# Kernel optimization log

Measured on AMD Instinct MI355X. Metric: run time of the kernel, lower is better.

Reference implementation:

```python
import jax, jax.numpy as jnp
import numpy as np
from jax import lax


def _lstm_layer(x, Wih, Whh, bih, bhh):
    # x: [B, T, D_in]; PyTorch gate order: i, f, g, o. Returns all hidden states [B, T, H].
    B = x.shape[0]
    H = Whh.shape[1]
    bias = bih + bhh
    # Precompute input projections for all timesteps: [T, B, 4H]
    xg = jnp.einsum('btd,gd->tbg', x, Wih) + bias

    def step(carry, xg_t):
        h, c = carry
        gates = xg_t + h @ Whh.T  # [B, 4H]
        i, f, g, o = jnp.split(gates, 4, axis=-1)
        i = jax.nn.sigmoid(i)
        f = jax.nn.sigmoid(f)
        g = jnp.tanh(g)
        o = jax.nn.sigmoid(o)
        c = f * c + i * g
        h = o * jnp.tanh(c)
        return (h, c), h

    h0 = jnp.zeros((B, H), dtype=x.dtype)
    c0 = jnp.zeros((B, H), dtype=x.dtype)
    (_, _), hs = lax.scan(step, (h0, c0), xg)  # hs: [T, B, H]
    return hs.transpose(1, 0, 2)


def setup_inputs() -> dict:
    key = jax.random.key(0)
    ks = jax.random.split(key, 13)
    B, T, D = 4096, 128, 32
    H1, H2 = 64, 32
    s = lambda n: 1.0 / np.sqrt(n)
    return {
        'x': jax.random.normal(ks[0], (B, T, D), jnp.float32),
        'Wih1': jax.random.uniform(ks[1], (4 * H1, D), jnp.float32, -s(H1), s(H1)),
        'Whh1': jax.random.uniform(ks[2], (4 * H1, H1), jnp.float32, -s(H1), s(H1)),
        'bih1': jax.random.uniform(ks[3], (4 * H1,), jnp.float32, -s(H1), s(H1)),
        'bhh1': jax.random.uniform(ks[4], (4 * H1,), jnp.float32, -s(H1), s(H1)),
        'Wih2': jax.random.uniform(ks[5], (4 * H2, H1), jnp.float32, -s(H2), s(H2)),
        'Whh2': jax.random.uniform(ks[6], (4 * H2, H2), jnp.float32, -s(H2), s(H2)),
        'bih2': jax.random.uniform(ks[7], (4 * H2,), jnp.float32, -s(H2), s(H2)),
        'bhh2': jax.random.uniform(ks[8], (4 * H2,), jnp.float32, -s(H2), s(H2)),
        'fc1_w': jax.random.uniform(ks[9], (16, H2), jnp.float32, -s(H2), s(H2)),
        'fc1_b': jax.random.uniform(ks[10], (16,), jnp.float32, -s(H2), s(H2)),
        'fc2_w': jax.random.uniform(ks[11], (1, 16), jnp.float32, -0.25, 0.25),
        'fc2_b': jax.random.uniform(ks[12], (1,), jnp.float32, -0.25, 0.25),
    }


def reference(x, Wih1, Whh1, bih1, bhh1, Wih2, Whh2, bih2, bhh2, fc1_w, fc1_b, fc2_w, fc2_b):
    out = _lstm_layer(x, Wih1, Whh1, bih1, bhh1)        # [B, T, H1]; dropout = identity (eval)
    out = _lstm_layer(out, Wih2, Whh2, bih2, bhh2)       # [B, T, H2]
    last = out[:, -1, :]                                  # [B, H2]
    h = jax.nn.relu(last @ fc1_w.T + fc1_b)               # [B, 16]
    return h @ fc2_w.T + fc2_b                            # [B, 1]
```

## Files before the change

kernel.cpp:

```cpp
#include <hip/hip_runtime.h>


constexpr int Tt      = 128;
constexpr int NB      = 8;
constexpr int THREADS = 256;

struct __align__(16) Smem {
  float scr[8192];
  float h1t[2][64][12];
  float h2t[2][32][12];
  float xs [2][32][12];
};

static_assert(sizeof(Smem) <= 80 * 1024, "need 2 blocks/CU");

__device__ __forceinline__ float frcp(float x)   { return __builtin_amdgcn_rcpf(x); }
__device__ __forceinline__ float fsig(float x)   { return frcp(1.0f + __expf(-x)); }
__device__ __forceinline__ float ftanh_(float x) { return 1.0f - 2.0f * frcp(1.0f + __expf(2.0f * x)); }

template<int P>
__device__ __forceinline__ float swz(float v) {
  return __int_as_float(__builtin_amdgcn_ds_swizzle(__float_as_int(v), P));
}

__global__ __launch_bounds__(THREADS, 2)
void lstm_fused(const float* __restrict__ x,
                const float* __restrict__ Wih1, const float* __restrict__ Whh1,
                const float* __restrict__ bih1, const float* __restrict__ bhh1,
                const float* __restrict__ Wih2, const float* __restrict__ Whh2,
                const float* __restrict__ bih2, const float* __restrict__ bhh2,
                const float* __restrict__ fc1w, const float* __restrict__ fc1b,
                const float* __restrict__ fc2w, const float* __restrict__ fc2b,
                float* __restrict__ out)
{
  __shared__ Smem s;
  const int tid = threadIdx.x;
  const int b0  = blockIdx.x * NB;

  const int ks1 = tid & 3;
  const int u1  = tid >> 2;
  const int ks2 = tid & 7;
  const int u2  = tid >> 3;

  float w1[24][4];
  float w2[12][4];

  auto stage = [&](const float* g, int n) {
    for (int e = tid * 4; e < n; e += THREADS * 4)
      *(float4*)&s.scr[e] = *(const float4*)&g[e];
  };

  stage(Wih1, 8192);
  __syncthreads();
#pragma unroll
  for (int j = 0; j < 8; ++j)
#pragma unroll
    for (int g = 0; g < 4; ++g)
      w1[j][g] = s.scr[(g * 64 + u1) * 32 + ks1 + 4 * j];
  __syncthreads();

  stage(Whh1, 8192);
  __syncthreads();
#pragma unroll
  for (int j = 8; j < 24; ++j)
#pragma unroll
    for (int g = 0; g < 2; ++g)
      w1[j][g] = s.scr[(g * 64 + u1) * 64 + ks1 + 4 * (j - 8)];
  __syncthreads();

  stage(Whh1 + 8192, 8192);
  __syncthreads();
#pragma unroll
  for (int j = 8; j < 24; ++j)
#pragma unroll
    for (int g = 2; g < 4; ++g)
      w1[j][g] = s.scr[((g - 2) * 64 + u1) * 64 + ks1 + 4 * (j - 8)];
  __syncthreads();

  stage(Wih2, 8192);
  __syncthreads();
#pragma unroll
  for (int j = 0; j < 8; ++j)
#pragma unroll
    for (int g = 0; g < 4; ++g)
      w2[j][g] = s.scr[(g * 32 + u2) * 64 + ks2 + 8 * j];
  __syncthreads();

  stage(Whh2, 4096);
  __syncthreads();
#pragma unroll
  for (int j = 8; j < 12; ++j)
#pragma unroll
    for (int g = 0; g < 4; ++g)
      w2[j][g] = s.scr[(g * 32 + u2) * 32 + ks2 + 8 * (j - 8)];

  float bias1[4], bias2[4];
#pragma unroll
  for (int g = 0; g < 4; ++g) {
    bias1[g] = bih1[g * 64 + u1] + bhh1[g * 64 + u1];
    bias2[g] = bih2[g * 32 + u2] + bhh2[g * 32 + u2];
  }

  for (int e = tid; e < 64 * 12; e += THREADS) (&s.h1t[0][0][0])[e] = 0.0f;
  for (int e = tid; e < 32 * 12; e += THREADS) (&s.h2t[0][0][0])[e] = 0.0f;

  const int    xb   = tid >> 5;
  const int    xd   = tid & 31;
  const float* xptr = x + (size_t)(b0 + xb) * (Tt * 32) + xd;
  s.xs[0][xd][xb] = xptr[0];

  float c1[2] = {0.0f, 0.0f};
  float c2    = 0.0f;

  const bool sA = (ks1 & 1) != 0;
  const bool sB = (ks1 & 2) != 0;
  const bool t0 = (ks2 & 1) != 0;
  const bool t1 = (ks2 & 2) != 0;
  const bool t2 = (ks2 & 4) != 0;

  __syncthreads();

#pragma unroll 1
  for (int t = 0; t < Tt; ++t) {
    const int c = t & 1, n = c ^ 1;

    float xpre = 0.0f;
    if (t + 1 < Tt) xpre = xptr[(size_t)(t + 1) * 32];

    float a[4][8];
#pragma unroll
    for (int g = 0; g < 4; ++g)
#pragma unroll
      for (int b = 0; b < 8; ++b) a[g][b] = 0.0f;

#pragma unroll
    for (int j = 0; j < 24; ++j) {
      const float* row = (j < 8) ? &s.xs[c][ks1 + 4 * j][0]
                                 : &s.h1t[c][ks1 + 4 * j - 32][0];
      float4 h0 = *(const float4*)&row[0];
      float4 h1 = *(const float4*)&row[4];
      float hv[8] = {h0.x, h0.y, h0.z, h0.w, h1.x, h1.y, h1.z, h1.w};
#pragma unroll
      for (int g = 0; g < 4; ++g)
#pragma unroll
        for (int b = 0; b < 8; ++b)
          a[g][b] = fmaf(w1[j][g], hv[b], a[g][b]);
    }

    float tot[4][2];
#pragma unroll
    for (int g = 0; g < 4; ++g) {
      float r1[4];
#pragma unroll
      for (int i = 0; i < 4; ++i) {
        float snd  = sA ? a[g][2 * i]     : a[g][2 * i + 1];
        float kept = sA ? a[g][2 * i + 1] : a[g][2 * i];
        r1[i] = kept + swz<0x041F>(snd);
      }
#pragma unroll
      for (int i = 0; i < 2; ++i) {
        float snd  = sB ? r1[2 * i]     : r1[2 * i + 1];
        float kept = sB ? r1[2 * i + 1] : r1[2 * i];
        tot[g][i] = kept + swz<0x081F>(snd);
      }
    }

#pragma unroll
    for (int bb = 0; bb < 2; ++bb) {
      float iv = fsig  (tot[0][bb] + bias1[0]);
      float fv = fsig  (tot[1][bb] + bias1[1]);
      float gv = ftanh_(tot[2][bb] + bias1[2]);
      float ov = fsig  (tot[3][bb] + bias1[3]);
      c1[bb] = fv * c1[bb] + iv * gv;
      s.h1t[n][u1][ks1 + 4 * bb] = ov * ftanh_(c1[bb]);
    }
    __syncthreads();

    if (t + 1 < Tt) s.xs[n][xd][xb] = xpre;

    float a2[4][8];
#pragma unroll
    for (int g = 0; g < 4; ++g)
#pragma unroll
      for (int b = 0; b < 8; ++b) a2[g][b] = 0.0f;

#pragma unroll
    for (int j = 0; j < 12; ++j) {
      const int k = ks2 + 8 * j;
      const float* row = (j < 8) ? &s.h1t[n][k][0] : &s.h2t[c][k - 64][0];
      float4 h0 = *(const float4*)&row[0];
      float4 h1 = *(const float4*)&row[4];
      float hv[8] = {h0.x, h0.y, h0.z, h0.w, h1.x, h1.y, h1.z, h1.w};
#pragma unroll
      for (int g = 0; g < 4; ++g)
#pragma unroll
        for (int b = 0; b < 8; ++b)
          a2[g][b] = fmaf(w2[j][g], hv[b], a2[g][b]);
    }

    float tot2[4];
#pragma unroll
    for (int g = 0; g < 4; ++g) {
      float r1[4];
#pragma unroll
      for (int i = 0; i < 4; ++i) {
        float snd  = t0 ? a2[g][2 * i]     : a2[g][2 * i + 1];
        float kept = t0 ? a2[g][2 * i + 1] : a2[g][2 * i];
        r1[i] = kept + swz<0x041F>(snd);
      }
      float r2[2];
#pragma unroll
      for (int i = 0; i < 2; ++i) {
        float snd  = t1 ? r1[2 * i]     : r1[2 * i + 1];
        float kept = t1 ? r1[2 * i + 1] : r1[2 * i];
        r2[i] = kept + swz<0x081F>(snd);
      }
      float snd  = t2 ? r2[0] : r2[1];
      float kept = t2 ? r2[1] : r2[0];
      tot2[g] = kept + swz<0x101F>(snd);
    }

    {
      float iv = fsig  (tot2[0] + bias2[0]);
      float fv = fsig  (tot2[1] + bias2[1]);
      float gv = ftanh_(tot2[2] + bias2[2]);
      float ov = fsig  (tot2[3] + bias2[3]);
      c2 = fv * c2 + iv * gv;
      s.h2t[n][u2][ks2] = ov * ftanh_(c2);
    }
    __syncthreads();
  }

  float* fc1out = s.scr;
  if (tid < 128) {
    const int fb = tid >> 4, fu = tid & 15;
    float sacc = fc1b[fu];
#pragma unroll
    for (int k = 0; k < 32; ++k)
      sacc = fmaf(fc1w[fu * 32 + k], s.h2t[0][k][fb], sacc);
    fc1out[fb * 16 + fu] = fmaxf(sacc, 0.0f);
  }
  __syncthreads();
  if (tid < NB) {
    float o = fc2b[0];
#pragma unroll
    for (int u = 0; u < 16; ++u) o = fmaf(fc2w[u], fc1out[tid * 16 + u], o);
    out[b0 + tid] = o;
  }
}

extern "C" void kernel_launch(void* const* d_in, const int* in_sizes, int n_in,
                              void* d_out, int out_size, void* d_ws, size_t ws_size,
                              hipStream_t stream) {
  const float* x    = (const float*)d_in[0];
  const float* Wih1 = (const float*)d_in[1];
  const float* Whh1 = (const float*)d_in[2];
  const float* bih1 = (const float*)d_in[3];
  const float* bhh1 = (const float*)d_in[4];
  const float* Wih2 = (const float*)d_in[5];
  const float* Whh2 = (const float*)d_in[6];
  const float* bih2 = (const float*)d_in[7];
  const float* bhh2 = (const float*)d_in[8];
  const float* fc1w = (const float*)d_in[9];
  const float* fc1b = (const float*)d_in[10];
  const float* fc2w = (const float*)d_in[11];
  const float* fc2b = (const float*)d_in[12];
  float* out = (float*)d_out;

  hipLaunchKernelGGL(lstm_fused, dim3(4096 / NB), dim3(THREADS), 0, stream,
                     x, Wih1, Whh1, bih1, bhh1,
                     Wih2, Whh2, bih2, bhh2,
                     fc1w, fc1b, fc2w, fc2b, out);
}
```

Measured before the change: 675.7 us.

## Use packed fp16 weights and hidden states with fdot2 in recurrent matvecs

Converts the per-thread register-resident weights and the shared-memory h/x tiles to packed half2, and replaces scalar fp32 FMAs with v_dot2 (fdot2) accumulating into fp32. This halves the FMA instruction count and LDS traffic per step in the latency-bound recurrence, and halves weight register usage. It risks accuracy loss from fp16 rounding of weights, inputs and hidden states accumulated across 128 timesteps.

```diff
diff --git a/kernel.cpp b/kernel.cpp
--- a/kernel.cpp
+++ b/kernel.cpp
@@ -1,5 +1,9 @@
 #include <hip/hip_runtime.h>
 
+
+typedef _Float16 f16;
+typedef f16 h2f __attribute__((ext_vector_type(2)));
+typedef f16 h8f __attribute__((ext_vector_type(8)));
 
 constexpr int Tt      = 128;
 constexpr int NB      = 8;
@@ -7,9 +11,9 @@
 
 struct __align__(16) Smem {
   float scr[8192];
-  float h1t[2][64][12];
-  float h2t[2][32][12];
-  float xs [2][32][12];
+  h2f h1p[2][32][8];
+  h2f h2p[2][16][8];
+  h2f xsp[2][16][8];
 };
 
 static_assert(sizeof(Smem) <= 80 * 1024, "need 2 blocks/CU");
@@ -21,6 +25,10 @@
 template<int P>
 __device__ __forceinline__ float swz(float v) {
   return __int_as_float(__builtin_amdgcn_ds_swizzle(__float_as_int(v), P));
+}
+
+__device__ __forceinline__ h2f pack2(float a, float b) {
+  h2f r; r[0] = (f16)a; r[1] = (f16)b; return r;
 }
 
 __global__ __launch_bounds__(THREADS, 2)
@@ -42,8 +50,8 @@
   const int ks2 = tid & 7;
   const int u2  = tid >> 3;
 
-  float w1[24][4];
-  float w2[12][4];
+  h2f w1[12][4];
+  h2f w2[6][4];
 
   auto stage = [&](const float* g, int n) {
     for (int e = tid * 4; e < n; e += THREADS * 4)
@@ -53,46 +61,61 @@
   stage(Wih1, 8192);
   __syncthreads();
 #pragma unroll
-  for (int j = 0; j < 8; ++j)
-#pragma unroll
-    for (int g = 0; g < 4; ++g)
-      w1[j][g] = s.scr[(g * 64 + u1) * 32 + ks1 + 4 * j];
+  for (int j = 0; j < 4; ++j) {
+    int col = 2 * (ks1 + 4 * j);
+#pragma unroll
+    for (int g = 0; g < 4; ++g)
+      w1[j][g] = pack2(s.scr[(g * 64 + u1) * 32 + col],
+                       s.scr[(g * 64 + u1) * 32 + col + 1]);
+  }
   __syncthreads();
 
   stage(Whh1, 8192);
   __syncthreads();
 #pragma unroll
-  for (int j = 8; j < 24; ++j)
+  for (int j = 4; j < 12; ++j) {
+    int col = 2 * (ks1 + 4 * j) - 32;
 #pragma unroll
     for (int g = 0; g < 2; ++g)
-      w1[j][g] = s.scr[(g * 64 + u1) * 64 + ks1 + 4 * (j - 8)];
+      w1[j][g] = pack2(s.scr[(g * 64 + u1) * 64 + col],
+                       s.scr[(g * 64 + u1) * 64 + col + 1]);
+  }
   __syncthreads();
 
   stage(Whh1 + 8192, 8192);
   __syncthreads();
 #pragma unroll
-  for (int j = 8; j < 24; ++j)
+  for (int j = 4; j < 12; ++j) {
+    int col = 2 * (ks1 + 4 * j) - 32;
 #pragma unroll
     for (int g = 2; g < 4; ++g)
-      w1[j][g] = s.scr[((g - 2) * 64 + u1) * 64 + ks1 + 4 * (j - 8)];
+      w1[j][g] = pack2(s.scr[((g - 2) * 64 + u1) * 64 + col],
+                       s.scr[((g - 2) * 64 + u1) * 64 + col + 1]);
+  }
   __syncthreads();
 
   stage(Wih2, 8192);
   __syncthreads();
 #pragma unroll
-  for (int j = 0; j < 8; ++j)
-#pragma unroll
-    for (int g = 0; g < 4; ++g)
-      w2[j][g] = s.scr[(g * 32 + u2) * 64 + ks2 + 8 * j];
+  for (int j = 0; j < 4; ++j) {
+    int col = 2 * (ks2 + 8 * j);
+#pragma unroll
+    for (int g = 0; g < 4; ++g)
+      w2[j][g] = pack2(s.scr[(g * 32 + u2) * 64 + col],
+                       s.scr[(g * 32 + u2) * 64 + col + 1]);
+  }
   __syncthreads();
 
   stage(Whh2, 4096);
   __syncthreads();
 #pragma unroll
-  for (int j = 8; j < 12; ++j)
-#pragma unroll
-    for (int g = 0; g < 4; ++g)
-      w2[j][g] = s.scr[(g * 32 + u2) * 32 + ks2 + 8 * (j - 8)];
+  for (int j = 4; j < 6; ++j) {
+    int col = 2 * (ks2 + 8 * j) - 64;
+#pragma unroll
+    for (int g = 0; g < 4; ++g)
+      w2[j][g] = pack2(s.scr[(g * 32 + u2) * 32 + col],
+                       s.scr[(g * 32 + u2) * 32 + col + 1]);
+  }
 
   float bias1[4], bias2[4];
 #pragma unroll
@@ -101,13 +124,22 @@
     bias2[g] = bih2[g * 32 + u2] + bhh2[g * 32 + u2];
   }
 
-  for (int e = tid; e < 64 * 12; e += THREADS) (&s.h1t[0][0][0])[e] = 0.0f;
-  for (int e = tid; e < 32 * 12; e += THREADS) (&s.h2t[0][0][0])[e] = 0.0f;
-
-  const int    xb   = tid >> 5;
-  const int    xd   = tid & 31;
-  const float* xptr = x + (size_t)(b0 + xb) * (Tt * 32) + xd;
-  s.xs[0][xd][xb] = xptr[0];
+  if (tid < 256) {
+    uint* z1 = (uint*)&s.h1p[0][0][0];
+    z1[tid] = 0u;
+  }
+  if (tid < 128) {
+    uint* z2 = (uint*)&s.h2p[0][0][0];
+    z2[tid] = 0u;
+  }
+
+  const int    xb   = tid >> 4;
+  const int    xr   = tid & 15;
+  const float* xptr = x + (size_t)(b0 + xb) * (Tt * 32) + 2 * xr;
+  if (tid < 128) {
+    float2 x0 = *(const float2*)xptr;
+    s.xsp[0][xr][xb] = pack2(x0.x, x0.y);
+  }
 
   float c1[2] = {0.0f, 0.0f};
   float c2    = 0.0f;
@@ -124,8 +156,8 @@
   for (int t = 0; t < Tt; ++t) {
     const int c = t & 1, n = c ^ 1;
 
-    float xpre = 0.0f;
-    if (t + 1 < Tt) xpre = xptr[(size_t)(t + 1) * 32];
+    float2 xpre = make_float2(0.0f, 0.0f);
+    if (tid < 128 && t + 1 < Tt) xpre = *(const float2*)(xptr + (size_t)(t + 1) * 32);
 
     float a[4][8];
 #pragma unroll
@@ -134,17 +166,21 @@
       for (int b = 0; b < 8; ++b) a[g][b] = 0.0f;
 
 #pragma unroll
-    for (int j = 0; j < 24; ++j) {
-      const float* row = (j < 8) ? &s.xs[c][ks1 + 4 * j][0]
-                                 : &s.h1t[c][ks1 + 4 * j - 32][0];
-      float4 h0 = *(const float4*)&row[0];
-      float4 h1 = *(const float4*)&row[4];
-      float hv[8] = {h0.x, h0.y, h0.z, h0.w, h1.x, h1.y, h1.z, h1.w};
-#pragma unroll
-      for (int g = 0; g < 4; ++g)
-#pragma unroll
-        for (int b = 0; b < 8; ++b)
-          a[g][b] = fmaf(w1[j][g], hv[b], a[g][b]);
+    for (int j = 0; j < 12; ++j) {
+      const h8f* row = (j < 4) ? (const h8f*)&s.xsp[c][ks1 + 4 * j][0]
+                               : (const h8f*)&s.h1p[c][ks1 + 4 * j - 16][0];
+      union { h8f v; h2f p[4]; } U0, U1;
+      U0.v = row[0];
+      U1.v = row[1];
+#pragma unroll
+      for (int g = 0; g < 4; ++g) {
+#pragma unroll
+        for (int b = 0; b < 4; ++b)
+          a[g][b] = __builtin_amdgcn_fdot2(w1[j][g], U0.p[b], a[g][b], false);
+#pragma unroll
+        for (int b = 0; b < 4; ++b)
+          a[g][4 + b] = __builtin_amdgcn_fdot2(w1[j][g], U1.p[b], a[g][4 + b], false);
+      }
     }
 
     float tot[4][2];
@@ -172,11 +208,13 @@
       float gv = ftanh_(tot[2][bb] + bias1[2]);
       float ov = fsig  (tot[3][bb] + bias1[3]);
       c1[bb] = fv * c1[bb] + iv * gv;
-      s.h1t[n][u1][ks1 + 4 * bb] = ov * ftanh_(c1[bb]);
+      float hval = ov * ftanh_(c1[bb]);
+      f16* dst = (f16*)&s.h1p[n][u1 >> 1][ks1 + 4 * bb];
+      dst[u1 & 1] = (f16)hval;
     }
     __syncthreads();
 
-    if (t + 1 < Tt) s.xs[n][xd][xb] = xpre;
+    if (tid < 128 && t + 1 < Tt) s.xsp[n][xr][xb] = pack2(xpre.x, xpre.y);
 
     float a2[4][8];
 #pragma unroll
@@ -185,17 +223,21 @@
       for (int b = 0; b < 8; ++b) a2[g][b] = 0.0f;
 
 #pragma unroll
-    for (int j = 0; j < 12; ++j) {
-      const int k = ks2 + 8 * j;
-      const float* row = (j < 8) ? &s.h1t[n][k][0] : &s.h2t[c][k - 64][0];
-      float4 h0 = *(const float4*)&row[0];
-      float4 h1 = *(const float4*)&row[4];
-      float hv[8] = {h0.x, h0.y, h0.z, h0.w, h1.x, h1.y, h1.z, h1.w};
-#pragma unroll
-      for (int g = 0; g < 4; ++g)
-#pragma unroll
-        for (int b = 0; b < 8; ++b)
-          a2[g][b] = fmaf(w2[j][g], hv[b], a2[g][b]);
+    for (int j = 0; j < 6; ++j) {
+      const h8f* row = (j < 4) ? (const h8f*)&s.h1p[n][ks2 + 8 * j][0]
+                               : (const h8f*)&s.h2p[c][ks2 + 8 * j - 32][0];
+      union { h8f v; h2f p[4]; } U0, U1;
+      U0.v = row[0];
+      U1.v = row[1];
+#pragma unroll
+      for (int g = 0; g < 4; ++g) {
+#pragma unroll
+        for (int b = 0; b < 4; ++b)
+          a2[g][b] = __builtin_amdgcn_fdot2(w2[j][g], U0.p[b], a2[g][b], false);
+#pragma unroll
+        for (int b = 0; b < 4; ++b)
+          a2[g][4 + b] = __builtin_amdgcn_fdot2(w2[j][g], U1.p[b], a2[g][4 + b], false);
+      }
     }
 
     float tot2[4];
@@ -226,7 +268,9 @@
       float gv = ftanh_(tot2[2] + bias2[2]);
       float ov = fsig  (tot2[3] + bias2[3]);
       c2 = fv * c2 + iv * gv;
-      s.h2t[n][u2][ks2] = ov * ftanh_(c2);
+      float hval = ov * ftanh_(c2);
+      f16* dst = (f16*)&s.h2p[n][u2 >> 1][ks2];
+      dst[u2 & 1] = (f16)hval;
     }
     __syncthreads();
   }
@@ -234,10 +278,13 @@
   float* fc1out = s.scr;
   if (tid < 128) {
     const int fb = tid >> 4, fu = tid & 15;
+    const f16* h2flat = (const f16*)&s.h2p[0][0][0];
     float sacc = fc1b[fu];
 #pragma unroll
-    for (int k = 0; k < 32; ++k)
-      sacc = fmaf(fc1w[fu * 32 + k], s.h2t[0][k][fb], sacc);
+    for (int k = 0; k < 32; ++k) {
+      float hv = (float)h2flat[(k >> 1) * 16 + fb * 2 + (k & 1)];
+      sacc = fmaf(fc1w[fu * 32 + k], hv, sacc);
+    }
     fc1out[fb * 16 + fu] = fmaxf(sacc, 0.0f);
   }
   __syncthreads();
```

Measured after the change: 638.0 us. 1.06x faster.
